# Kernel optimization log

Hardware: AMD Instinct MI355X
Metric: run time of the kernel (lower is better)

The kernel has to match this reference:

```python
import jax, jax.numpy as jnp
import numpy as np

D_MODEL = 768
D_STATE = 16
K_CONV = 4
BATCH = 2
SEQ = 2048


def setup_inputs() -> dict:
    key = jax.random.key(0)
    ks = jax.random.split(key, 16)
    dm, ds, K = D_MODEL, D_STATE, K_CONV
    s = 0.02
    inp = {
        "x": jax.random.normal(ks[0], (BATCH, SEQ, dm), dtype=jnp.float32),
        # linear weights stored (in, out); y = x @ W + b (equivalent to torch Linear)
        "Wi": jax.random.normal(ks[1], (dm, 2 * dm), dtype=jnp.float32) * s,
        "bi": jnp.zeros((2 * dm,), jnp.float32),
        "Wconv": jax.random.normal(ks[2], (dm, K), dtype=jnp.float32) * s,
        "bconv": jnp.zeros((dm,), jnp.float32),
        "Wdt": jax.random.normal(ks[3], (dm, dm), dtype=jnp.float32) * s,
        "bdt": jnp.zeros((dm,), jnp.float32),
        "WB": jax.random.normal(ks[4], (dm, dm * ds), dtype=jnp.float32) * s,
        "bB": jnp.zeros((dm * ds,), jnp.float32),
        "WC": jax.random.normal(ks[5], (dm, dm * ds), dtype=jnp.float32) * s,
        "bC": jnp.zeros((dm * ds,), jnp.float32),
        "A_log": jnp.zeros((dm, ds), jnp.float32),  # matches nn.Parameter(torch.zeros)
        "D": jnp.ones((dm,), jnp.float32),          # matches nn.Parameter(torch.ones)
        "Wo": jax.random.normal(ks[6], (dm, dm), dtype=jnp.float32) * s,
        "bo": jnp.zeros((dm,), jnp.float32),
    }
    return inp


def _forward(x, Wi, bi, Wconv, bconv, Wdt, bdt, WB, bB, WC, bC, A_log, D, Wo, bo):
    B, L, dm = x.shape
    ds = A_log.shape[1]
    K = Wconv.shape[1]

    uv = x @ Wi + bi                        # (B, L, 2*dm)
    u, v = uv[..., :dm], uv[..., dm:]

    # causal depthwise conv1d: torch pads K-1 both sides, keeps first L outputs
    u_pad = jnp.pad(u, ((0, 0), (K - 1, 0), (0, 0)))
    u_conv = bconv + sum(u_pad[:, k:k + L, :] * Wconv[:, k] for k in range(K))

    dt = jax.nn.softplus(u_conv @ Wdt + bdt)            # (B, L, dm)
    Bt = (u_conv @ WB + bB).reshape(B, L, dm, ds)       # (B, L, dm, ds)
    Ct = (u_conv @ WC + bC).reshape(B, L, dm, ds)
    A = -jnp.exp(A_log)                                  # (dm, ds)

    def step(s, inputs):
        dt_t, u_t, B_tt, C_tt = inputs                   # (B,dm), (B,dm), (B,dm,ds), (B,dm,ds)
        dt_e = dt_t[..., None]
        s = s * jnp.exp(dt_e * A) + dt_e * B_tt * u_t[..., None]
        y = jnp.sum(C_tt * s, axis=-1) + D * u_t         # (B, dm)
        return s, y

    s0 = jnp.zeros((B, dm, ds), x.dtype)
    xs = (dt.transpose(1, 0, 2), u_conv.transpose(1, 0, 2),
          Bt.transpose(1, 0, 2, 3), Ct.transpose(1, 0, 2, 3))
    _, ys = jax.lax.scan(step, s0, xs)                   # ys: (L, B, dm)
    y = ys.transpose(1, 0, 2)

    y = y * jax.nn.sigmoid(v)
    return y @ Wo + bo


def reference(x, Wi, bi, Wconv, bconv, Wdt, bdt, WB, bB, WC, bC, A_log, D, Wo, bo):
    return _forward(x, Wi, bi, Wconv, bconv, Wdt, bdt, WB, bB, WC, bC, A_log, D, Wo, bo)
```

## Files before the change

### kernel.cpp

```cpp
#include <hip/hip_runtime.h>

#define DM 768
#define DS 16
#define SEQ 2048
#define BATCH 2
#define MROWS (BATCH*SEQ)
#define N_UV (2*DM)
#define N_BC (DM*DS)
#define NGRP (BATCH*DM/4)
#define SUBMAX 64

typedef _Float16 half8 __attribute__((ext_vector_type(8)));
typedef float floatx4 __attribute__((ext_vector_type(4)));

static __device__ __forceinline__ unsigned short f2h(float f) {
  _Float16 h = (_Float16)f;
  return __builtin_bit_cast(unsigned short, h);
}
static __device__ __forceinline__ float h2f(unsigned short u) {
  return (float)__builtin_bit_cast(_Float16, u);
}
static __device__ __forceinline__ float softplus_f(float x) {
  return (x > 20.f) ? x : log1pf(__expf(x));
}
static __device__ __forceinline__ void async_cp16(const unsigned short* g,
                                                  unsigned short* l) {
  __builtin_amdgcn_global_load_lds(
      (const __attribute__((address_space(1))) void*)g,
      (__attribute__((address_space(3))) void*)l, 16, 0, 0);
}
static __device__ __forceinline__ float row_reduce16(float v) {
  int x;
  x = __builtin_amdgcn_update_dpp(0, __builtin_bit_cast(int, v), 0x128, 0xf, 0xf, true);
  v += __builtin_bit_cast(float, x);
  x = __builtin_amdgcn_update_dpp(0, __builtin_bit_cast(int, v), 0x124, 0xf, 0xf, true);
  v += __builtin_bit_cast(float, x);
  x = __builtin_amdgcn_update_dpp(0, __builtin_bit_cast(int, v), 0x122, 0xf, 0xf, true);
  v += __builtin_bit_cast(float, x);
  x = __builtin_amdgcn_update_dpp(0, __builtin_bit_cast(int, v), 0x121, 0xf, 0xf, true);
  v += __builtin_bit_cast(float, x);
  return v;
}

__global__ void convert_f2h(const float* __restrict__ in,
                            unsigned short* __restrict__ out, int n) {
  int i = (blockIdx.x * blockDim.x + threadIdx.x) * 4;
  if (i >= n) return;
  float4 f = *(const float4*)(in + i);
  ushort4 h;
  h.x = f2h(f.x); h.y = f2h(f.y); h.z = f2h(f.z); h.w = f2h(f.w);
  *(ushort4*)(out + i) = h;
}

__global__ void transpose_w5(const float* __restrict__ W0, const float* __restrict__ W1,
                             const float* __restrict__ W2, const float* __restrict__ W3,
                             const float* __restrict__ W4,
                             unsigned short* __restrict__ T0, unsigned short* __restrict__ T1,
                             unsigned short* __restrict__ T2, unsigned short* __restrict__ T3,
                             unsigned short* __restrict__ T4,
                             int N0, int N1, int N2, int N3, int N4) {
  const float* W; unsigned short* WT; int N;
  switch (blockIdx.z) {
    case 0: W = W0; WT = T0; N = N0; break;
    case 1: W = W1; WT = T1; N = N1; break;
    case 2: W = W2; WT = T2; N = N2; break;
    case 3: W = W3; WT = T3; N = N3; break;
    default: W = W4; WT = T4; N = N4; break;
  }
  int n0 = blockIdx.x * 32;
  if (n0 >= N) return;
  int k0 = blockIdx.y * 32;
  __shared__ float tile[32][33];
  int tx = threadIdx.x, ty = threadIdx.y;
#pragma unroll
  for (int i = 0; i < 32; i += 8)
    tile[ty + i][tx] = W[(size_t)(k0 + ty + i) * N + (n0 + tx)];
  __syncthreads();
  int kp = tx & 15, half = tx >> 4;
#pragma unroll
  for (int i = 0; i < 2; i++) {
    int nl = ty + half * 8 + i * 16;
    unsigned int pk = (unsigned int)f2h(tile[2 * kp][nl]) |
                      ((unsigned int)f2h(tile[2 * kp + 1][nl]) << 16);
    *(unsigned int*)&WT[(size_t)(n0 + nl) * DM + k0 + 2 * kp] = pk;
  }
}

template<int ACT, int OUTH>
__global__ __launch_bounds__(256)
void gemm_f16(const unsigned short* __restrict__ A,
              const unsigned short* __restrict__ BT0,
              const unsigned short* __restrict__ BT1,
              const float* __restrict__ bias0,
              const float* __restrict__ bias1,
              void* __restrict__ Cout0,
              void* __restrict__ Cout1,
              int M, int N, int K, int TCa, int bstride, int row0) {
  const unsigned short* BT = blockIdx.z ? BT1 : BT0;
  const float* bias = blockIdx.z ? bias1 : bias0;
  void* Cout = blockIdx.z ? Cout1 : Cout0;
  __shared__ __align__(16) unsigned short As[128 * 32];
  __shared__ __align__(16) unsigned short Bs[128 * 32];
  const int m0 = blockIdx.y * 128, n0 = blockIdx.x * 128;
  const int tid = threadIdx.x;
  const int lane = tid & 63, wave = tid >> 6;
  const int wm = (wave >> 1) * 64, wn = (wave & 1) * 64;
  const int l16 = lane & 15, quad = lane >> 4;
  const int sr = tid >> 2;
  const int sc = (((tid & 3) ^ ((tid >> 3) & 3))) * 8;
  const int pch = (quad ^ ((l16 >> 1) & 3)) * 8;

  floatx4 acc[4][4] = {};

  const int mA0 = m0 + sr, mA1 = m0 + sr + 64;
  const int gA0 = (mA0 / TCa) * bstride + row0 + (mA0 % TCa);
  const int gA1 = (mA1 / TCa) * bstride + row0 + (mA1 % TCa);
  const unsigned short* Arow0 = A + (size_t)gA0 * K + sc;
  const unsigned short* Arow1 = A + (size_t)gA1 * K + sc;
  const unsigned short* Brow0 = BT + (size_t)(n0 + sr) * K + sc;
  const unsigned short* Brow1 = BT + (size_t)(n0 + sr + 64) * K + sc;
  unsigned short* ldsA0 = As + (wave * 16) * 32;
  unsigned short* ldsA1 = As + (64 + wave * 16) * 32;
  unsigned short* ldsB0 = Bs + (wave * 16) * 32;
  unsigned short* ldsB1 = Bs + (64 + wave * 16) * 32;

  for (int k0 = 0; k0 < K; k0 += 32) {
    async_cp16(Arow0 + k0, ldsA0);
    async_cp16(Arow1 + k0, ldsA1);
    async_cp16(Brow0 + k0, ldsB0);
    async_cp16(Brow1 + k0, ldsB1);
    __syncthreads();
    half8 af[4], bf[4];
#pragma unroll
    for (int i = 0; i < 4; i++) {
      af[i] = __builtin_bit_cast(half8, *(const uint4*)&As[(wm + i * 16 + l16) * 32 + pch]);
      bf[i] = __builtin_bit_cast(half8, *(const uint4*)&Bs[(wn + i * 16 + l16) * 32 + pch]);
    }
#pragma unroll
    for (int mi = 0; mi < 4; mi++)
#pragma unroll
      for (int ni = 0; ni < 4; ni++)
        acc[mi][ni] = __builtin_amdgcn_mfma_f32_16x16x32_f16(af[mi], bf[ni], acc[mi][ni], 0, 0, 0);
    __syncthreads();
  }

#pragma unroll
  for (int ni = 0; ni < 4; ni++) {
    int col = n0 + wn + ni * 16 + l16;
    float bv = bias[col];
#pragma unroll
    for (int mi = 0; mi < 4; mi++) {
#pragma unroll
      for (int r = 0; r < 4; r++) {
        int row = m0 + wm + mi * 16 + quad * 4 + r;
        float v = acc[mi][ni][r] + bv;
        if (ACT == 1) v = softplus_f(v);
        if (OUTH) ((unsigned short*)Cout)[(size_t)row * N + col] = f2h(v);
        else      ((float*)Cout)[(size_t)row * N + col] = v;
      }
    }
  }
}

__global__ void dwconv(const unsigned short* __restrict__ uv,
                       const float* __restrict__ Wconv,
                       const float* __restrict__ bconv,
                       unsigned short* __restrict__ uc) {
  int idx = blockIdx.x * 256 + threadIdx.x;
  int c = (idx % (DM / 2)) * 2;
  int row = idx / (DM / 2);
  int t = row & (SEQ - 1);
  float a0 = bconv[c], a1 = bconv[c + 1];
  const float* w0 = Wconv + c * 4;
  const float* w1 = Wconv + (c + 1) * 4;
#pragma unroll
  for (int k = 0; k < 4; k++) {
    int tt = t - 3 + k;
    if (tt >= 0) {
      ushort2 u2 = *(const ushort2*)&uv[(size_t)(row - 3 + k) * N_UV + c];
      a0 += h2f(u2.x) * w0[k];
      a1 += h2f(u2.y) * w1[k];
    }
  }
  ushort2 o; o.x = f2h(a0); o.y = f2h(a1);
  *(ushort2*)&uc[(size_t)row * DM + c] = o;
}

__global__ __launch_bounds__(64)
void scan_pass1(const unsigned short* __restrict__ dt,
                const unsigned short* __restrict__ uc,
                const unsigned short* __restrict__ Btc,
                const float* __restrict__ A_log,
                float* __restrict__ Ssub,
                float* __restrict__ Aexp,
                int ci, int TC, int SUBn) {
  const int TSUB = TC / SUBn;
  int wid = blockIdx.x, sub = blockIdx.y;
  int b = wid / (DM / 4);
  int c0 = (wid % (DM / 4)) * 4;
  int lane = threadIdx.x;
  int c = c0 + (lane >> 4);
  float Acj = -__expf(A_log[c0 * DS + lane]);
  int col = c0 * DS + lane;
  size_t gbase = (size_t)b * SEQ + (size_t)ci * TC + (size_t)sub * TSUB;
  size_t lbase = (size_t)b * TC + (size_t)sub * TSUB;

  float s = 0.f, dsum = 0.f;
  float n_dt[8], n_u[8], n_B[8];
#pragma unroll
  for (int i = 0; i < 8; i++) {
    n_dt[i] = h2f(dt[(gbase + i) * DM + c]);
    n_u[i]  = h2f(uc[(gbase + i) * DM + c]);
    n_B[i]  = h2f(Btc[(lbase + i) * N_BC + col]);
  }
  for (int t0 = 0; t0 < TSUB; t0 += 8) {
    float c_dt[8], c_u[8], c_B[8];
#pragma unroll
    for (int i = 0; i < 8; i++) { c_dt[i] = n_dt[i]; c_u[i] = n_u[i]; c_B[i] = n_B[i]; }
    if (t0 + 8 < TSUB) {
#pragma unroll
      for (int i = 0; i < 8; i++) {
        size_t gr = gbase + t0 + 8 + i, lr = lbase + t0 + 8 + i;
        n_dt[i] = h2f(dt[gr * DM + c]);
        n_u[i]  = h2f(uc[gr * DM + c]);
        n_B[i]  = h2f(Btc[lr * N_BC + col]);
      }
    }
#pragma unroll
    for (int i = 0; i < 8; i++) {
      float dtc = c_dt[i];
      dsum += dtc;
      float a = __expf(dtc * Acj);
      s = fmaf(s, a, dtc * c_B[i] * c_u[i]);
    }
  }
  int idx = (sub * BATCH + b) * N_BC + col;
  Ssub[idx] = s;
  Aexp[idx] = __expf(Acj * dsum);
}

template<int SUBN>
__global__ __launch_bounds__(64)
void scan_combine(const float* Ssub, const float* Aexp,
                  float* Sinit, float* s_state, int ci) {
  int wid = blockIdx.x;
  int b = wid / (DM / 4);
  int c0 = (wid % (DM / 4)) * 4;
  int col = c0 * DS + threadIdx.x;
  int sidx = b * N_BC + col;
  float sa[SUBN], ae[SUBN];
#pragma unroll
  for (int k = 0; k < SUBN; k++) {
    int idx = (k * BATCH + b) * N_BC + col;
    sa[k] = Ssub[idx];
    ae[k] = Aexp[idx];
  }
  float s = (ci == 0) ? 0.f : s_state[sidx];
#pragma unroll
  for (int k = 0; k < SUBN; k++) {
    int idx = (k * BATCH + b) * N_BC + col;
    Sinit[idx] = s;
    s = fmaf(s, ae[k], sa[k]);
  }
  s_state[sidx] = s;
}

__global__ __launch_bounds__(64)
void scan_pass2(const unsigned short* __restrict__ dt,
                const unsigned short* __restrict__ uc,
                const unsigned short* __restrict__ Btc,
                const unsigned short* __restrict__ Ctc,
                const unsigned short* __restrict__ uv,
                const float* __restrict__ A_log,
                const float* __restrict__ Dv,
                const float* __restrict__ Sinit,
                unsigned short* __restrict__ yg,
                int ci, int TC, int SUBn) {
  const int TSUB = TC / SUBn;
  int wid = blockIdx.x, sub = blockIdx.y;
  int b = wid / (DM / 4);
  int c0 = (wid % (DM / 4)) * 4;
  int lane = threadIdx.x;
  int j = lane & 15;
  int c = c0 + (lane >> 4);
  float Acj = -__expf(A_log[c0 * DS + lane]);
  float Dc = Dv[c];
  int col = c0 * DS + lane;
  float s = Sinit[(sub * BATCH + b) * N_BC + col];
  size_t gbase = (size_t)b * SEQ + (size_t)ci * TC + (size_t)sub * TSUB;
  size_t lbase = (size_t)b * TC + (size_t)sub * TSUB;

  float n_dt[8], n_u[8], n_B[8], n_C[8], n_v[8];
#pragma unroll
  for (int i = 0; i < 8; i++) {
    size_t gr = gbase + i, lr = lbase + i;
    n_dt[i] = h2f(dt[gr * DM + c]);
    n_u[i]  = h2f(uc[gr * DM + c]);
    n_B[i]  = h2f(Btc[lr * N_BC + col]);
    n_C[i]  = h2f(Ctc[lr * N_BC + col]);
    n_v[i]  = h2f(uv[gr * N_UV + DM + c]);
  }
  for (int t0 = 0; t0 < TSUB; t0 += 8) {
    float c_dt[8], c_u[8], c_B[8], c_C[8], c_v[8];
#pragma unroll
    for (int i = 0; i < 8; i++) {
      c_dt[i] = n_dt[i]; c_u[i] = n_u[i]; c_B[i] = n_B[i];
      c_C[i] = n_C[i]; c_v[i] = n_v[i];
    }
    if (t0 + 8 < TSUB) {
#pragma unroll
      for (int i = 0; i < 8; i++) {
        size_t gr = gbase + t0 + 8 + i, lr = lbase + t0 + 8 + i;
        n_dt[i] = h2f(dt[gr * DM + c]);
        n_u[i]  = h2f(uc[gr * DM + c]);
        n_B[i]  = h2f(Btc[lr * N_BC + col]);
        n_C[i]  = h2f(Ctc[lr * N_BC + col]);
        n_v[i]  = h2f(uv[gr * N_UV + DM + c]);
      }
    }
#pragma unroll
    for (int i = 0; i < 8; i++) {
      float dtc = c_dt[i];
      float a = __expf(dtc * Acj);
      s = fmaf(s, a, dtc * c_B[i] * c_u[i]);
      float yt = row_reduce16(c_C[i] * s);
      if (j == 0) {
        float y = yt + Dc * c_u[i];
        float g = 1.f / (1.f + __expf(-c_v[i]));
        yg[(gbase + t0 + i) * DM + c] = f2h(y * g);
      }
    }
  }
}

extern "C" void kernel_launch(void* const* d_in, const int* in_sizes, int n_in,
                              void* d_out, int out_size, void* d_ws, size_t ws_size,
                              hipStream_t stream) {
  const float* x     = (const float*)d_in[0];
  const float* Wi    = (const float*)d_in[1];
  const float* bi    = (const float*)d_in[2];
  const float* Wconv = (const float*)d_in[3];
  const float* bconv = (const float*)d_in[4];
  const float* Wdt   = (const float*)d_in[5];
  const float* bdt   = (const float*)d_in[6];
  const float* WB    = (const float*)d_in[7];
  const float* bB    = (const float*)d_in[8];
  const float* WC    = (const float*)d_in[9];
  const float* bC    = (const float*)d_in[10];
  const float* A_log = (const float*)d_in[11];
  const float* Dv    = (const float*)d_in[12];
  const float* Wo    = (const float*)d_in[13];
  const float* bo    = (const float*)d_in[14];
  float* out = (float*)d_out;
  (void)in_sizes; (void)n_in; (void)out_size;

  auto pad = [](size_t b) { return (b + 255) & ~(size_t)255; };

  const size_t sz_xb   = pad((size_t)MROWS * DM * 2);
  const size_t sz_WiT  = pad((size_t)N_UV * DM * 2);
  const size_t sz_WdtT = pad((size_t)DM * DM * 2);
  const size_t sz_WBT  = pad((size_t)N_BC * DM * 2);
  const size_t sz_WCT  = pad((size_t)N_BC * DM * 2);
  const size_t sz_WoT  = pad((size_t)DM * DM * 2);
  const size_t sz_uvb  = pad((size_t)MROWS * N_UV * 2);
  const size_t sz_ucb  = pad((size_t)MROWS * DM * 2);
  const size_t sz_dtb  = pad((size_t)MROWS * DM * 2);
  const size_t sz_st   = pad((size_t)BATCH * N_BC * 4);
  const size_t sz_sub  = pad((size_t)SUBMAX * BATCH * N_BC * 4);
  const size_t fixed = sz_xb + sz_WiT + sz_WdtT + sz_WBT + sz_WCT + sz_WoT +
                       sz_uvb + sz_ucb + sz_dtb + sz_st + 2 * sz_sub;

  int NC = 16;
  for (int nc : {1, 2, 4, 8, 16}) {
    size_t need = fixed + 2 * pad((size_t)BATCH * (SEQ / nc) * N_BC * 2);
    if (need <= ws_size) { NC = nc; break; }
  }
  const int TC = SEQ / NC;
  const int MC = BATCH * TC;
  const int SUBn = (TC / 8 < SUBMAX) ? (TC / 8) : SUBMAX;

  char* ws = (char*)d_ws;
  size_t off = 0;
  auto alloc = [&](size_t bytes) { char* p = ws + off; off += bytes; return p; };
  unsigned short* xb   = (unsigned short*)alloc(sz_xb);
  unsigned short* WiT  = (unsigned short*)alloc(sz_WiT);
  unsigned short* WdtT = (unsigned short*)alloc(sz_WdtT);
  unsigned short* WBT  = (unsigned short*)alloc(sz_WBT);
  unsigned short* WCT  = (unsigned short*)alloc(sz_WCT);
  unsigned short* WoT  = (unsigned short*)alloc(sz_WoT);
  unsigned short* uvb  = (unsigned short*)alloc(sz_uvb);
  unsigned short* ucb  = (unsigned short*)alloc(sz_ucb);
  unsigned short* dtb  = (unsigned short*)alloc(sz_dtb);
  float*          sst  = (float*)alloc(sz_st);
  float*          Ssub = (float*)alloc(sz_sub);
  float*          Aexp = (float*)alloc(sz_sub);
  unsigned short* Btc  = (unsigned short*)alloc(pad((size_t)MC * N_BC * 2));
  unsigned short* Ctc  = (unsigned short*)alloc(pad((size_t)MC * N_BC * 2));
  unsigned short* ygb  = xb;
  float*          Sini = Ssub;

  convert_f2h<<<dim3(MROWS * DM / 1024), dim3(256), 0, stream>>>(x, xb, MROWS * DM);
  transpose_w5<<<dim3(N_BC / 32, DM / 32, 5), dim3(32, 8), 0, stream>>>(
      Wi, Wdt, WB, WC, Wo, WiT, WdtT, WBT, WCT, WoT, N_UV, DM, N_BC, N_BC, DM);

  gemm_f16<0, 1><<<dim3(N_UV / 128, MROWS / 128, 1), 256, 0, stream>>>(
      xb, WiT, WiT, bi, bi, uvb, uvb, MROWS, N_UV, DM, MROWS, 0, 0);
  dwconv<<<dim3(MROWS * DM / 512), 256, 0, stream>>>(uvb, Wconv, bconv, ucb);
  gemm_f16<1, 1><<<dim3(DM / 128, MROWS / 128, 1), 256, 0, stream>>>(
      ucb, WdtT, WdtT, bdt, bdt, dtb, dtb, MROWS, DM, DM, MROWS, 0, 0);

  for (int ci = 0; ci < NC; ci++) {
    gemm_f16<0, 1><<<dim3(N_BC / 128, MC / 128, 2), 256, 0, stream>>>(
        ucb, WBT, WCT, bB, bC, Btc, Ctc, MC, N_BC, DM, TC, SEQ, ci * TC);
    scan_pass1<<<dim3(NGRP, SUBn), 64, 0, stream>>>(dtb, ucb, Btc, A_log,
                                                    Ssub, Aexp, ci, TC, SUBn);
    switch (SUBn) {
      case 64: scan_combine<64><<<dim3(NGRP), 64, 0, stream>>>(Ssub, Aexp, Sini, sst, ci); break;
      case 32: scan_combine<32><<<dim3(NGRP), 64, 0, stream>>>(Ssub, Aexp, Sini, sst, ci); break;
      default: scan_combine<16><<<dim3(NGRP), 64, 0, stream>>>(Ssub, Aexp, Sini, sst, ci); break;
    }
    scan_pass2<<<dim3(NGRP, SUBn), 64, 0, stream>>>(dtb, ucb, Btc, Ctc, uvb,
                                                    A_log, Dv, Sini, ygb, ci, TC, SUBn);
  }

  gemm_f16<0, 0><<<dim3(DM / 128, MROWS / 128, 1), 256, 0, stream>>>(
      ygb, WoT, WoT, bo, bo, out, out, MROWS, DM, DM, MROWS, 0, 0);
}
```

Measured before the change: 604.7 us.

## Quantize B/C projection GEMM to int8 with per-row scales

Adds a per-row symmetric int8 quantization kernel for the conv output activations and the transposed WB/WC weights, and a new int8 MFMA GEMM (16x16x64 i8) that dequantizes with row and column scales in the epilogue. This replaces the fp16 GEMM for the large Bt/Ct projections, which dominate the FLOPs, aiming to double MFMA throughput and halve operand bytes. It adds quantization passes and int8 rounding error on the activations feeding the scan, which risks accuracy.

Result: faster. 553.6 us (-8.5%).

```diff
diff --git a/kernel.cpp b/kernel.cpp
--- a/kernel.cpp
+++ b/kernel.cpp
@@ -12,6 +12,9 @@
 
 typedef _Float16 half8 __attribute__((ext_vector_type(8)));
 typedef float floatx4 __attribute__((ext_vector_type(4)));
+typedef int i32x4 __attribute__((ext_vector_type(4)));
+typedef unsigned short us8 __attribute__((ext_vector_type(8)));
+typedef signed char c8 __attribute__((ext_vector_type(8)));
 
 static __device__ __forceinline__ unsigned short f2h(float f) {
   _Float16 h = (_Float16)f;
@@ -23,8 +26,7 @@
 static __device__ __forceinline__ float softplus_f(float x) {
   return (x > 20.f) ? x : log1pf(__expf(x));
 }
-static __device__ __forceinline__ void async_cp16(const unsigned short* g,
-                                                  unsigned short* l) {
+static __device__ __forceinline__ void async_cp16(const void* g, void* l) {
   __builtin_amdgcn_global_load_lds(
       (const __attribute__((address_space(1))) void*)g,
       (__attribute__((address_space(3))) void*)l, 16, 0, 0);
@@ -84,6 +86,46 @@
                       ((unsigned int)f2h(tile[2 * kp + 1][nl]) << 16);
     *(unsigned int*)&WT[(size_t)(n0 + nl) * DM + k0 + 2 * kp] = pk;
   }
+}
+
+__global__ __launch_bounds__(256)
+void quant_rows(const unsigned short* __restrict__ in0,
+                const unsigned short* __restrict__ in1,
+                signed char* __restrict__ out0, signed char* __restrict__ out1,
+                float* __restrict__ sc0, float* __restrict__ sc1, int R) {
+  const unsigned short* in = blockIdx.y ? in1 : in0;
+  signed char* out = blockIdx.y ? out1 : out0;
+  float* scp = blockIdx.y ? sc1 : sc0;
+  int row = blockIdx.x * 4 + (threadIdx.x >> 6);
+  if (row >= R) return;
+  int lane = threadIdx.x & 63;
+  const us8* ch = (const us8*)(in + (size_t)row * DM);
+  us8 a = ch[lane];
+  us8 b = ch[64 + (lane & 31)];
+  float fa[8], fb[8];
+  float m = 0.f;
+#pragma unroll
+  for (int j = 0; j < 8; j++) { fa[j] = h2f(a[j]); m = fmaxf(m, fabsf(fa[j])); }
+#pragma unroll
+  for (int j = 0; j < 8; j++) fb[j] = h2f(b[j]);
+  if (lane < 32) {
+#pragma unroll
+    for (int j = 0; j < 8; j++) m = fmaxf(m, fabsf(fb[j]));
+  }
+#pragma unroll
+  for (int off = 32; off; off >>= 1) m = fmaxf(m, __shfl_xor(m, off));
+  float inv = (m > 0.f) ? 127.f / m : 0.f;
+  if (lane == 0) scp[row] = m * (1.f / 127.f);
+  c8 qa, qb;
+#pragma unroll
+  for (int j = 0; j < 8; j++)
+    qa[j] = (signed char)__float2int_rn(fminf(fmaxf(fa[j] * inv, -127.f), 127.f));
+#pragma unroll
+  for (int j = 0; j < 8; j++)
+    qb[j] = (signed char)__float2int_rn(fminf(fmaxf(fb[j] * inv, -127.f), 127.f));
+  c8* o = (c8*)(out + (size_t)row * DM);
+  o[lane] = qa;
+  if (lane < 32) o[64 + lane] = qb;
 }
 
 template<int ACT, int OUTH>
@@ -157,6 +199,92 @@
         if (ACT == 1) v = softplus_f(v);
         if (OUTH) ((unsigned short*)Cout)[(size_t)row * N + col] = f2h(v);
         else      ((float*)Cout)[(size_t)row * N + col] = v;
+      }
+    }
+  }
+}
+
+__global__ __launch_bounds__(256)
+void gemm_i8(const signed char* __restrict__ A,
+             const signed char* __restrict__ BT0,
+             const signed char* __restrict__ BT1,
+             const float* __restrict__ bias0,
+             const float* __restrict__ bias1,
+             const float* __restrict__ sA,
+             const float* __restrict__ sB0,
+             const float* __restrict__ sB1,
+             unsigned short* __restrict__ C0,
+             unsigned short* __restrict__ C1,
+             int M, int N, int K, int TCa, int bstride, int row0) {
+  const signed char* BT = blockIdx.z ? BT1 : BT0;
+  const float* bias = blockIdx.z ? bias1 : bias0;
+  const float* sB = blockIdx.z ? sB1 : sB0;
+  unsigned short* Cout = blockIdx.z ? C1 : C0;
+  __shared__ __align__(16) signed char As[128 * 64];
+  __shared__ __align__(16) signed char Bs[128 * 64];
+  const int m0 = blockIdx.y * 128, n0 = blockIdx.x * 128;
+  const int tid = threadIdx.x;
+  const int lane = tid & 63, wave = tid >> 6;
+  const int wm = (wave >> 1) * 64, wn = (wave & 1) * 64;
+  const int l16 = lane & 15, quad = lane >> 4;
+  const int sr = tid >> 2;
+  const int sc = ((tid & 3) ^ ((tid >> 3) & 3)) * 16;
+  const int pch = (quad ^ ((l16 >> 1) & 3)) * 16;
+
+  i32x4 acc[4][4] = {};
+
+  const int mA0 = m0 + sr, mA1 = m0 + sr + 64;
+  const int gA0 = (mA0 / TCa) * bstride + row0 + (mA0 % TCa);
+  const int gA1 = (mA1 / TCa) * bstride + row0 + (mA1 % TCa);
+  const signed char* Arow0 = A + (size_t)gA0 * K + sc;
+  const signed char* Arow1 = A + (size_t)gA1 * K + sc;
+  const signed char* Brow0 = BT + (size_t)(n0 + sr) * K + sc;
+  const signed char* Brow1 = BT + (size_t)(n0 + sr + 64) * K + sc;
+  signed char* ldsA0 = As + (wave * 16) * 64;
+  signed char* ldsA1 = As + (64 + wave * 16) * 64;
+  signed char* ldsB0 = Bs + (wave * 16) * 64;
+  signed char* ldsB1 = Bs + (64 + wave * 16) * 64;
+
+  for (int k0 = 0; k0 < K; k0 += 64) {
+    async_cp16(Arow0 + k0, ldsA0);
+    async_cp16(Arow1 + k0, ldsA1);
+    async_cp16(Brow0 + k0, ldsB0);
+    async_cp16(Brow1 + k0, ldsB1);
+    __syncthreads();
+    i32x4 af[4], bf[4];
+#pragma unroll
+    for (int i = 0; i < 4; i++) {
+      af[i] = *(const i32x4*)&As[(wm + i * 16 + l16) * 64 + pch];
+      bf[i] = *(const i32x4*)&Bs[(wn + i * 16 + l16) * 64 + pch];
+    }
+#pragma unroll
+    for (int mi = 0; mi < 4; mi++)
+#pragma unroll
+      for (int ni = 0; ni < 4; ni++)
+        acc[mi][ni] = __builtin_amdgcn_mfma_i32_16x16x64_i8(af[mi], bf[ni], acc[mi][ni], 0, 0, 0);
+    __syncthreads();
+  }
+
+  const int rowAbase = (m0 / TCa) * (bstride - TCa) + row0;
+  float savs[4][4];
+#pragma unroll
+  for (int mi = 0; mi < 4; mi++)
+#pragma unroll
+    for (int r = 0; r < 4; r++)
+      savs[mi][r] = sA[rowAbase + m0 + wm + mi * 16 + quad * 4 + r];
+
+#pragma unroll
+  for (int ni = 0; ni < 4; ni++) {
+    int col = n0 + wn + ni * 16 + l16;
+    float bv = bias[col];
+    float sbv = sB[col];
+#pragma unroll
+    for (int mi = 0; mi < 4; mi++) {
+#pragma unroll
+      for (int r = 0; r < 4; r++) {
+        int row = m0 + wm + mi * 16 + quad * 4 + r;
+        float v = (float)acc[mi][ni][r] * (savs[mi][r] * sbv) + bv;
+        Cout[(size_t)row * N + col] = f2h(v);
       }
     }
   }
@@ -367,8 +495,13 @@
   const size_t sz_dtb  = pad((size_t)MROWS * DM * 2);
   const size_t sz_st   = pad((size_t)BATCH * N_BC * 4);
   const size_t sz_sub  = pad((size_t)SUBMAX * BATCH * N_BC * 4);
+  const size_t sz_uc8  = pad((size_t)MROWS * DM);
+  const size_t sz_w8   = pad((size_t)N_BC * DM);
+  const size_t sz_sA   = pad((size_t)MROWS * 4);
+  const size_t sz_sB   = pad((size_t)N_BC * 4);
   const size_t fixed = sz_xb + sz_WiT + sz_WdtT + sz_WBT + sz_WCT + sz_WoT +
-                       sz_uvb + sz_ucb + sz_dtb + sz_st + 2 * sz_sub;
+                       sz_uvb + sz_ucb + sz_dtb + sz_st + 2 * sz_sub +
+                       sz_uc8 + 2 * sz_w8 + sz_sA + 2 * sz_sB;
 
   int NC = 16;
   for (int nc : {1, 2, 4, 8, 16}) {
@@ -394,6 +527,12 @@
   float*          sst  = (float*)alloc(sz_st);
   float*          Ssub = (float*)alloc(sz_sub);
   float*          Aexp = (float*)alloc(sz_sub);
+  signed char*    uc8  = (signed char*)alloc(sz_uc8);
+  signed char*    WBT8 = (signed char*)alloc(sz_w8);
+  signed char*    WCT8 = (signed char*)alloc(sz_w8);
+  float*          sAu  = (float*)alloc(sz_sA);
+  float*          sB0  = (float*)alloc(sz_sB);
+  float*          sB1  = (float*)alloc(sz_sB);
   unsigned short* Btc  = (unsigned short*)alloc(pad((size_t)MC * N_BC * 2));
   unsigned short* Ctc  = (unsigned short*)alloc(pad((size_t)MC * N_BC * 2));
   unsigned short* ygb  = xb;
@@ -402,16 +541,21 @@
   convert_f2h<<<dim3(MROWS * DM / 1024), dim3(256), 0, stream>>>(x, xb, MROWS * DM);
   transpose_w5<<<dim3(N_BC / 32, DM / 32, 5), dim3(32, 8), 0, stream>>>(
       Wi, Wdt, WB, WC, Wo, WiT, WdtT, WBT, WCT, WoT, N_UV, DM, N_BC, N_BC, DM);
+  quant_rows<<<dim3(N_BC / 4, 2), 256, 0, stream>>>(WBT, WCT, WBT8, WCT8,
+                                                    sB0, sB1, N_BC);
 
   gemm_f16<0, 1><<<dim3(N_UV / 128, MROWS / 128, 1), 256, 0, stream>>>(
       xb, WiT, WiT, bi, bi, uvb, uvb, MROWS, N_UV, DM, MROWS, 0, 0);
   dwconv<<<dim3(MROWS * DM / 512), 256, 0, stream>>>(uvb, Wconv, bconv, ucb);
+  quant_rows<<<dim3(MROWS / 4, 1), 256, 0, stream>>>(ucb, ucb, uc8, uc8,
+                                                     sAu, sAu, MROWS);
   gemm_f16<1, 1><<<dim3(DM / 128, MROWS / 128, 1), 256, 0, stream>>>(
       ucb, WdtT, WdtT, bdt, bdt, dtb, dtb, MROWS, DM, DM, MROWS, 0, 0);
 
   for (int ci = 0; ci < NC; ci++) {
-    gemm_f16<0, 1><<<dim3(N_BC / 128, MC / 128, 2), 256, 0, stream>>>(
-        ucb, WBT, WCT, bB, bC, Btc, Ctc, MC, N_BC, DM, TC, SEQ, ci * TC);
+    gemm_i8<<<dim3(N_BC / 128, MC / 128, 2), 256, 0, stream>>>(
+        uc8, WBT8, WCT8, bB, bC, sAu, sB0, sB1, Btc, Ctc,
+        MC, N_BC, DM, TC, SEQ, ci * TC);
     scan_pass1<<<dim3(NGRP, SUBn), 64, 0, stream>>>(dtb, ucb, Btc, A_log,
                                                     Ssub, Aexp, ci, TC, SUBn);
     switch (SUBn) {
```
